# Kernel optimization log

Measured on AMD Instinct MI355X. Metric: run time of the kernel, lower is better.

## Reference

```python
import jax, jax.numpy as jnp
import numpy as np

N = 50000      # num nodes
E = 800000     # num edges (before self loops)
B = 50         # num graphs in batch
F_IN = 15
C = 64         # hidden_channels
H = 4          # num_heads
NEG_SLOPE = 0.2  # PyG GATConv default


def setup_inputs() -> dict:
    key = jax.random.key(0)
    ks = jax.random.split(key, 32)
    s = 0.05
    inp = {
        "x": jax.random.normal(ks[0], (N, F_IN), dtype=jnp.float32),
        "edge_index": jax.random.randint(ks[1], (2, E), 0, N, dtype=jnp.int32),
        "batch": jnp.sort(jax.random.randint(ks[2], (N,), 0, B, dtype=jnp.int32)),
        "W1": jax.random.normal(ks[3], (F_IN, H * C)) * s,
        "aS1": jax.random.normal(ks[4], (H, C)) * s,
        "aD1": jax.random.normal(ks[5], (H, C)) * s,
        "b1": jnp.zeros((H * C,)),
        "W2": jax.random.normal(ks[6], (H * C, H * C)) * s,
        "aS2": jax.random.normal(ks[7], (H, C)) * s,
        "aD2": jax.random.normal(ks[8], (H, C)) * s,
        "b2": jnp.zeros((H * C,)),
        # GAT layer 3: 256 -> 64, 1 head
        "W3": jax.random.normal(ks[9], (H * C, C)) * s,
        "aS3": jax.random.normal(ks[10], (1, C)) * s,
        "aD3": jax.random.normal(ks[11], (1, C)) * s,
        "b3": jnp.zeros((C,)),
        # node attention MLP: 64 -> 32 -> 1
        "Wna1": jax.random.normal(ks[12], (C, 32)) * s,
        "bna1": jnp.zeros((32,)),
        "Wna2": jax.random.normal(ks[13], (32, 1)) * s,
        "bna2": jnp.zeros((1,)),
        # graph classifier: 128 -> 128 -> 64 -> 1
        "Wc1": jax.random.normal(ks[14], (2 * C, 128)) * s,
        "bc1": jnp.zeros((128,)),
        "Wc2": jax.random.normal(ks[15], (128, 64)) * s,
        "bc2": jnp.zeros((64,)),
        "Wc3": jax.random.normal(ks[16], (64, 1)) * s,
        "bc3": jnp.zeros((1,)),
    }
    return inp


def _gat_conv(x, src, dst, W, a_src, a_dst, b, heads, ch):
    """PyG-style GATConv (add_self_loops=True, negative_slope=0.2, eval mode)."""
    n = x.shape[0]
    h = (x @ W).reshape(n, heads, ch)               # [N, H, C]
    alpha_s = jnp.einsum('nhc,hc->nh', h, a_src)    # per-node src score
    alpha_d = jnp.einsum('nhc,hc->nh', h, a_dst)
    loops = jnp.arange(n, dtype=src.dtype)
    s = jnp.concatenate([src, loops])               # [E+N]
    d = jnp.concatenate([dst, loops])
    e = jax.nn.leaky_relu(alpha_s[s] + alpha_d[d], NEG_SLOPE)   # [E+N, H]
    # segment softmax over incoming edges of each dst node
    m = jax.ops.segment_max(e, d, num_segments=n)
    ex = jnp.exp(e - m[d])
    denom = jax.ops.segment_sum(ex, d, num_segments=n)
    alpha = ex / denom[d]                           # [E+N, H]
    msg = h[s] * alpha[:, :, None]                  # [E+N, H, C]
    out = jax.ops.segment_sum(msg, d, num_segments=n)  # [N, H, C]
    return out.reshape(n, heads * ch) + b


def reference(x, edge_index, batch, W1, aS1, aD1, b1, W2, aS2, aD2, b2,
              W3, aS3, aD3, b3, Wna1, bna1, Wna2, bna2,
              Wc1, bc1, Wc2, bc2, Wc3, bc3):
    src, dst = edge_index[0], edge_index[1]
    x1 = jax.nn.elu(_gat_conv(x, src, dst, W1, aS1, aD1, b1, H, C))
    x2 = jax.nn.elu(_gat_conv(x1, src, dst, W2, aS2, aD2, b2, H, C))
    x3 = jax.nn.elu(_gat_conv(x2, src, dst, W3, aS3, aD3, b3, 1, C))  # [N, 64]

    # node attention: MLP then softmax over ALL nodes (dim=0, as in source)
    na = jax.nn.relu(x3 @ Wna1 + bna1) @ Wna2 + bna2   # [N, 1]
    node_attention = jax.nn.softmax(na, axis=0)

    # graph pooling
    ones = jnp.ones((x3.shape[0],), dtype=x3.dtype)
    cnt = jax.ops.segment_sum(ones, batch, num_segments=B)         # [B]
    mean = jax.ops.segment_sum(x3, batch, num_segments=B) / jnp.maximum(cnt, 1.0)[:, None]
    mx = jax.ops.segment_max(x3, batch, num_segments=B)
    mx = jnp.where(cnt[:, None] > 0, mx, 0.0)
    g = jnp.concatenate([mean, mx], axis=1)                        # [B, 128]

    h1 = jax.nn.relu(g @ Wc1 + bc1)
    h2 = jax.nn.relu(h1 @ Wc2 + bc2)
    risk = jax.nn.sigmoid(h2 @ Wc3 + bc3)                          # [B, 1]
    return (risk, node_attention)
```

## Files before the change

### kernel.cpp

```cpp
#include <hip/hip_runtime.h>
#include <math.h>

#define NN 50000
#define NP 50176
#define EE 800000
#define ETOT (EE + NN)
#define BB 50
#define PC 16

typedef unsigned short u16;
typedef unsigned char u8;
typedef __attribute__((ext_vector_type(8))) short short8;
typedef __attribute__((ext_vector_type(4))) float floatx4;
typedef __attribute__((ext_vector_type(2))) float floatx2;

__device__ __forceinline__ float b2f(u16 u) {
  return __int_as_float(((int)u) << 16);
}
__device__ __forceinline__ u16 f2b(float f) {
  unsigned u = __float_as_uint(f);
  unsigned r = (u + 0x7fffu + ((u >> 16) & 1u)) >> 16;
  return (u16)r;
}
__device__ __forceinline__ u8 f2f8(float v) {
  return (u8)(__builtin_amdgcn_cvt_pk_fp8_f32(v, v, 0, false) & 0xFF);
}
__device__ __forceinline__ float readlane_f(float v, int l) {
  return __int_as_float(__builtin_amdgcn_readlane(__float_as_int(v), l));
}
__device__ __forceinline__ float blo(unsigned w) { return __uint_as_float(w << 16); }
__device__ __forceinline__ float bhi(unsigned w) { return __uint_as_float(w & 0xffff0000u); }

__global__ void count_kernel(const int* __restrict__ ei, int* __restrict__ cnt) {
  int e = blockIdx.x * blockDim.x + threadIdx.x;
  if (e >= ETOT) return;
  int d = (e < EE) ? ei[EE + e] : (e - EE);
  atomicAdd(&cnt[d], 1);
}

__global__ void scan1_kernel(const int* __restrict__ cnt, int* __restrict__ rowp,
                             int* __restrict__ part) {
  __shared__ int s[512];
  int t = threadIdx.x;
  int i = blockIdx.x * 512 + t;
  int v = (i < NN) ? cnt[i] : 0;
  s[t] = v;
  __syncthreads();
  for (int off = 1; off < 512; off <<= 1) {
    int add = (t >= off) ? s[t - off] : 0;
    __syncthreads();
    s[t] += add;
    __syncthreads();
  }
  if (i < NN) rowp[i] = s[t] - v;
  if (t == 511) part[blockIdx.x] = s[511];
}

__global__ void scan2_kernel(int* __restrict__ part, int* __restrict__ rowp) {
  __shared__ int s[128];
  int t = threadIdx.x;
  int v = (t < 98) ? part[t] : 0;
  s[t] = v;
  __syncthreads();
  for (int off = 1; off < 128; off <<= 1) {
    int add = (t >= off) ? s[t - off] : 0;
    __syncthreads();
    s[t] += add;
    __syncthreads();
  }
  if (t < 98) part[t] = s[t] - v;
  if (t == 97) rowp[NN] = s[97];
}

__global__ void scan3_kernel(int* __restrict__ rowp, const int* __restrict__ part) {
  int i = blockIdx.x * 512 + threadIdx.x;
  if (i < NN) rowp[i] += part[blockIdx.x];
}

__global__ void fill_kernel(const int* __restrict__ ei, const int* __restrict__ rowp,
                            int* __restrict__ cur, int* __restrict__ col) {
  int e = blockIdx.x * blockDim.x + threadIdx.x;
  if (e >= ETOT) return;
  int s, d;
  if (e < EE) { s = ei[e]; d = ei[EE + e]; } else { s = e - EE; d = s; }
  int p = atomicAdd(&cur[d], 1);
  col[rowp[d] + p] = s;
}

__global__ void prep_kernel(const float* __restrict__ x, const float* __restrict__ W1,
                            const float* __restrict__ W2, const float* __restrict__ W3,
                            u16* __restrict__ xb, u16* __restrict__ W1t,
                            u16* __restrict__ W2t, u16* __restrict__ W3t) {
  const int T0 = NP * 32, T1 = T0 + 8192, T2 = T1 + 65536, T3 = T2 + 16384;
  int i = blockIdx.x * 256 + threadIdx.x;
  if (i < T0) {
    int n = i >> 5, c = i & 31;
    xb[i] = (n < NN && c < 15) ? f2b(x[n * 15 + c]) : (u16)0;
  } else if (i < T1) {
    int j = i - T0, n = j >> 5, k = j & 31;
    W1t[j] = (k < 15) ? f2b(W1[k * 256 + n]) : (u16)0;
  } else if (i < T2) {
    int j = i - T1, n = j >> 8, k = j & 255;
    W2t[j] = f2b(W2[k * 256 + n]);
  } else if (i < T3) {
    int j = i - T2, n = j >> 8, k = j & 255;
    W3t[j] = f2b(W3[k * 64 + n]);
  }
}

template <int BK, bool F8>
__global__ __launch_bounds__(256) void gemm_bf16_kernel(
    const u16* __restrict__ A, const u16* __restrict__ Bt, u16* __restrict__ C,
    u8* __restrict__ C8, int K, int N, const float* __restrict__ aS,
    const float* __restrict__ aD, float* __restrict__ as_o,
    float* __restrict__ ad_o, int Hh) {
  __shared__ u16 Al[128][BK + 8];
  __shared__ u16 Bl[64][BK + 8];
  __shared__ float sS[4][64], sD[4][64];
  int R0 = blockIdx.x * 128, C0 = blockIdx.y * 64;
  int wid = threadIdx.x >> 6, lane = threadIdx.x & 63;
  int wr = (wid >> 1) * 64, wc = (wid & 1) * 32;
  int lrow = lane & 15, lk8 = (lane >> 4) * 8;
  int rq = (lane >> 4) * 4;
  const int Q4 = BK / 4;
  const int nA = 128 * Q4, nB = 64 * Q4;
  floatx4 acc[4][2];
#pragma unroll
  for (int i = 0; i < 4; ++i)
#pragma unroll
    for (int j = 0; j < 2; ++j) acc[i][j] = (floatx4){0.f, 0.f, 0.f, 0.f};

  for (int k0 = 0; k0 < K; k0 += BK) {
    for (int c = threadIdx.x; c < nA + nB; c += 256) {
      if (c < nA) {
        int r = c / Q4, o = (c % Q4) * 4;
        *(ushort4*)&Al[r][o] = *(const ushort4*)&A[(size_t)(R0 + r) * K + k0 + o];
      } else {
        int c2 = c - nA;
        int r = c2 / Q4, o = (c2 % Q4) * 4;
        *(ushort4*)&Bl[r][o] = *(const ushort4*)&Bt[(size_t)(C0 + r) * K + k0 + o];
      }
    }
    __syncthreads();
#pragma unroll
    for (int ks = 0; ks < BK / 32; ++ks) {
      short8 a[4], b[2];
#pragma unroll
      for (int i = 0; i < 4; ++i) a[i] = *(const short8*)&Al[wr + i * 16 + lrow][ks * 32 + lk8];
#pragma unroll
      for (int j = 0; j < 2; ++j) b[j] = *(const short8*)&Bl[wc + j * 16 + lrow][ks * 32 + lk8];
#pragma unroll
      for (int i = 0; i < 4; ++i)
#pragma unroll
        for (int j = 0; j < 2; ++j)
          acc[i][j] = __builtin_amdgcn_mfma_f32_16x16x32_bf16(a[i], b[j], acc[i][j], 0, 0, 0);
    }
    __syncthreads();
  }
#pragma unroll
  for (int i = 0; i < 4; ++i)
#pragma unroll
    for (int j = 0; j < 2; ++j)
#pragma unroll
      for (int q = 0; q < 4; ++q) {
        int gr = R0 + wr + i * 16 + rq + q;
        int gc = C0 + wc + j * 16 + lrow;
        if constexpr (F8)
          C8[(size_t)gr * N + gc] = f2f8(acc[i][j][q]);
        else
          C[(size_t)gr * N + gc] = f2b(acc[i][j][q]);
      }
  int hb = blockIdx.y * 64;
  float wS0 = aS[hb + wc + lrow], wS1 = aS[hb + wc + 16 + lrow];
  float wD0 = aD[hb + wc + lrow], wD1 = aD[hb + wc + 16 + lrow];
#pragma unroll
  for (int i = 0; i < 4; ++i)
#pragma unroll
    for (int q = 0; q < 4; ++q) {
      float vS = acc[i][0][q] * wS0 + acc[i][1][q] * wS1;
      float vD = acc[i][0][q] * wD0 + acc[i][1][q] * wD1;
#pragma unroll
      for (int o = 8; o; o >>= 1) {
        vS += __shfl_xor(vS, o, 64);
        vD += __shfl_xor(vD, o, 64);
      }
      if (lrow == 0) {
        int rl = i * 16 + rq + q;
        sS[wid][rl] = vS;
        sD[wid][rl] = vD;
      }
    }
  __syncthreads();
  if (threadIdx.x < 128) {
    int p = threadIdx.x >> 6, r = threadIdx.x & 63;
    int gr = R0 + p * 64 + r;
    as_o[(size_t)gr * Hh + blockIdx.y] = sS[2 * p][r] + sS[2 * p + 1][r];
    ad_o[(size_t)gr * Hh + blockIdx.y] = sD[2 * p][r] + sD[2 * p + 1][r];
  }
}

__global__ __launch_bounds__(256) void agg4_kernel(
    const u8* __restrict__ h8, const float* __restrict__ as_i,
    const float* __restrict__ ad_i, const int* __restrict__ rowp,
    const int* __restrict__ col, const float* __restrict__ bias,
    u16* __restrict__ xo) {
  __shared__ float exs[4][64][4];
  int wid = threadIdx.x >> 6, lane = threadIdx.x & 63;
  int d = blockIdx.x * 4 + wid;
  int rp0 = rowp[d], deg = rowp[d + 1] - rp0;
  float4 add = *(const float4*)&ad_i[(size_t)d * 4];
  int hj = lane >> 4;
  int lq = lane << 2;
  float acc0 = 0.f, acc1 = 0.f, acc2 = 0.f, acc3 = 0.f;
  float den0 = 0.f, den1 = 0.f, den2 = 0.f, den3 = 0.f;

  for (int base = 0; base < deg; base += 64) {
    int i = base + lane;
    bool valid = i < deg;
    int s = valid ? col[rp0 + i] : 0;
    float4 asv = *(const float4*)&as_i[(size_t)s * 4];
    float e0 = asv.x + add.x, e1 = asv.y + add.y, e2 = asv.z + add.z, e3 = asv.w + add.w;
    e0 = (e0 > 0.f) ? e0 : 0.2f * e0;
    e1 = (e1 > 0.f) ? e1 : 0.2f * e1;
    e2 = (e2 > 0.f) ? e2 : 0.2f * e2;
    e3 = (e3 > 0.f) ? e3 : 0.2f * e3;
    float x0 = valid ? __expf(e0) : 0.f;
    float x1 = valid ? __expf(e1) : 0.f;
    float x2 = valid ? __expf(e2) : 0.f;
    float x3 = valid ? __expf(e3) : 0.f;
    den0 += x0; den1 += x1; den2 += x2; den3 += x3;
    *(float4*)&exs[wid][lane][0] = make_float4(x0, x1, x2, x3);
    __threadfence_block();
    int cnt = min(64, deg - base);
    int k8 = cnt & ~7;
    for (int k = 0; k < k8; k += 8) {
      unsigned wv[8];
      float qv[8];
#pragma unroll
      for (int u = 0; u < 8; ++u) {
        int sk = __builtin_amdgcn_readlane(s, k + u);
        qv[u] = exs[wid][k + u][hj];
        wv[u] = *(const unsigned*)&h8[(size_t)sk * 256 + lq];
      }
#pragma unroll
      for (int u = 0; u < 8; ++u) {
        floatx2 lo = __builtin_amdgcn_cvt_pk_f32_fp8(wv[u], false);
        floatx2 hi = __builtin_amdgcn_cvt_pk_f32_fp8(wv[u], true);
        acc0 += qv[u] * lo.x;
        acc1 += qv[u] * lo.y;
        acc2 += qv[u] * hi.x;
        acc3 += qv[u] * hi.y;
      }
    }
    for (int k = k8; k < cnt; ++k) {
      int sk = __builtin_amdgcn_readlane(s, k);
      float qk = exs[wid][k][hj];
      unsigned wv = *(const unsigned*)&h8[(size_t)sk * 256 + lq];
      floatx2 lo = __builtin_amdgcn_cvt_pk_f32_fp8(wv, false);
      floatx2 hi = __builtin_amdgcn_cvt_pk_f32_fp8(wv, true);
      acc0 += qk * lo.x;
      acc1 += qk * lo.y;
      acc2 += qk * hi.x;
      acc3 += qk * hi.y;
    }
  }
#pragma unroll
  for (int o = 32; o; o >>= 1) {
    den0 += __shfl_xor(den0, o, 64);
    den1 += __shfl_xor(den1, o, 64);
    den2 += __shfl_xor(den2, o, 64);
    den3 += __shfl_xor(den3, o, 64);
  }
  float den = (hj == 0) ? den0 : (hj == 1) ? den1 : (hj == 2) ? den2 : den3;
  float inv = 1.f / den;
  float4 bv = *(const float4*)&bias[lq];
  float v0 = acc0 * inv + bv.x;
  float v1 = acc1 * inv + bv.y;
  float v2 = acc2 * inv + bv.z;
  float v3 = acc3 * inv + bv.w;
  v0 = (v0 > 0.f) ? v0 : expm1f(v0);
  v1 = (v1 > 0.f) ? v1 : expm1f(v1);
  v2 = (v2 > 0.f) ? v2 : expm1f(v2);
  v3 = (v3 > 0.f) ? v3 : expm1f(v3);
  ushort4 o4;
  o4.x = f2b(v0); o4.y = f2b(v1); o4.z = f2b(v2); o4.w = f2b(v3);
  ((ushort4*)xo)[(size_t)d * 64 + lane] = o4;
}

__global__ __launch_bounds__(256) void agg1_kernel(
    const u16* __restrict__ h, const float* __restrict__ as_i,
    const float* __restrict__ ad_i, const int* __restrict__ rowp,
    const int* __restrict__ col, const float* __restrict__ bias,
    float* __restrict__ xo) {
  int wid = threadIdx.x >> 6, lane = threadIdx.x & 63;
  int d = blockIdx.x * 4 + wid;
  int rp0 = rowp[d], deg = rowp[d + 1] - rp0;
  float add = ad_i[d];
  float acc = 0.f, den = 0.f;
  for (int base = 0; base < deg; base += 64) {
    int i = base + lane;
    bool valid = i < deg;
    int s = valid ? col[rp0 + i] : 0;
    float e = as_i[s] + add;
    e = (e > 0.f) ? e : 0.2f * e;
    float ex = valid ? __expf(e) : 0.f;
    den += ex;
    int cnt = min(64, deg - base);
    int k8 = cnt & ~7;
    for (int k = 0; k < k8; k += 8) {
      int sA[8];
      float qA[8], hv[8];
#pragma unroll
      for (int u = 0; u < 8; ++u) {
        sA[u] = __builtin_amdgcn_readlane(s, k + u);
        qA[u] = readlane_f(ex, k + u);
      }
#pragma unroll
      for (int u = 0; u < 8; ++u) hv[u] = b2f(h[(size_t)sA[u] * 64 + lane]);
      float p0 = qA[0] * hv[0] + qA[1] * hv[1];
      float p1 = qA[2] * hv[2] + qA[3] * hv[3];
      float p2 = qA[4] * hv[4] + qA[5] * hv[5];
      float p3 = qA[6] * hv[6] + qA[7] * hv[7];
      acc += (p0 + p1) + (p2 + p3);
    }
    for (int k = k8; k < cnt; ++k) {
      int sk = __builtin_amdgcn_readlane(s, k);
      float qk = readlane_f(ex, k);
      acc += qk * b2f(h[(size_t)sk * 64 + lane]);
    }
  }
#pragma unroll
  for (int o = 32; o; o >>= 1) den += __shfl_xor(den, o, 64);
  float v = acc / den + bias[lane];
  v = (v > 0.f) ? v : expm1f(v);
  xo[(size_t)d * 64 + lane] = v;
}

__global__ void na_kernel(const float* __restrict__ x3, const float* __restrict__ W1,
                          const float* __restrict__ b1, const float* __restrict__ W2,
                          const float* __restrict__ b2, float* __restrict__ na,
                          float* __restrict__ gsum) {
  __shared__ float Ws[64 * 32];
  __shared__ float W2s[32];
  __shared__ float sred[4];
  for (int i = threadIdx.x; i < 2048; i += blockDim.x) Ws[i] = W1[i];
  if (threadIdx.x < 32) W2s[threadIdx.x] = W2[threadIdx.x];
  __syncthreads();
  int n = blockIdx.x * blockDim.x + threadIdx.x;
  float ez = 0.f;
  if (n < NN) {
    float hid[32];
#pragma unroll
    for (int j = 0; j < 32; ++j) hid[j] = b1[j];
    const float4* x4 = (const float4*)&x3[(size_t)n * 64];
    for (int kk = 0; kk < 16; ++kk) {
      float4 xv = x4[kk];
#pragma unroll
      for (int j = 0; j < 32; ++j) {
        hid[j] += xv.x * Ws[(kk * 4 + 0) * 32 + j];
        hid[j] += xv.y * Ws[(kk * 4 + 1) * 32 + j];
        hid[j] += xv.z * Ws[(kk * 4 + 2) * 32 + j];
        hid[j] += xv.w * Ws[(kk * 4 + 3) * 32 + j];
      }
    }
    float z = b2[0];
#pragma unroll
    for (int j = 0; j < 32; ++j) z += fmaxf(hid[j], 0.f) * W2s[j];
    ez = __expf(z);
    na[n] = ez;
  }
  float acc = ez;
  for (int o = 32; o; o >>= 1) acc += __shfl_xor(acc, o, 64);
  int wid = threadIdx.x >> 6, lane = threadIdx.x & 63;
  if (lane == 0) sred[wid] = acc;
  __syncthreads();
  if (threadIdx.x == 0) atomicAdd(gsum, sred[0] + sred[1] + sred[2] + sred[3]);
}

__global__ void na_write_kernel(const float* __restrict__ na, const float* __restrict__ gsum,
                                float* __restrict__ out) {
  int n = blockIdx.x * blockDim.x + threadIdx.x;
  if (n >= NN) return;
  out[n] = na[n] / gsum[0];
}

__global__ void pool1_kernel(const float* __restrict__ x3, const int* __restrict__ batch,
                             float* __restrict__ ppsum, float* __restrict__ ppmax) {
  int b = blockIdx.x, c = blockIdx.y;
  int lane = threadIdx.x & 63, wid = threadIdx.x >> 6;
  int lo = 0, hi = NN;
  while (lo < hi) { int m = (lo + hi) >> 1; if (batch[m] < b) lo = m + 1; else hi = m; }
  int start = lo;
  lo = start; hi = NN;
  while (lo < hi) { int m = (lo + hi) >> 1; if (batch[m] < b + 1) lo = m + 1; else hi = m; }
  int end = lo;
  int len = end - start;
  int c0 = start + (int)((long)len * c / PC);
  int c1 = start + (int)((long)len * (c + 1) / PC);
  float acc = 0.f, mx = -INFINITY;
  for (int n = c0 + wid; n < c1; n += 4) {
    float v = x3[(size_t)n * 64 + lane];
    acc += v;
    mx = fmaxf(mx, v);
  }
  __shared__ float ssum[4][64], smax[4][64];
  ssum[wid][lane] = acc;
  smax[wid][lane] = mx;
  __syncthreads();
  if (wid == 0) {
    acc = ssum[0][lane] + ssum[1][lane] + ssum[2][lane] + ssum[3][lane];
    mx = fmaxf(fmaxf(smax[0][lane], smax[1][lane]), fmaxf(smax[2][lane], smax[3][lane]));
    size_t o = ((size_t)c * BB + b) * 64 + lane;
    ppsum[o] = acc;
    ppmax[o] = mx;
  }
}

__global__ void pool2cls_kernel(const float* __restrict__ ppsum, const float* __restrict__ ppmax,
                                const int* __restrict__ batch, const float* __restrict__ Wc1,
                                const float* __restrict__ bc1, const float* __restrict__ Wc2,
                                const float* __restrict__ bc2, const float* __restrict__ Wc3,
                                const float* __restrict__ bc3, float* __restrict__ out) {
  __shared__ float g[128], h1[128], h2[64], scnt;
  int b = blockIdx.x, t = threadIdx.x;
  if (t == 0) {
    int lo = 0, hi = NN;
    while (lo < hi) { int m = (lo + hi) >> 1; if (batch[m] < b) lo = m + 1; else hi = m; }
    int start = lo;
    lo = start; hi = NN;
    while (lo < hi) { int m = (lo + hi) >> 1; if (batch[m] < b + 1) lo = m + 1; else hi = m; }
    scnt = (float)(lo - start);
  }
  float s = 0.f, m = -INFINITY;
  if (t < 64) {
#pragma unroll
    for (int c = 0; c < PC; ++c) {
      size_t o = ((size_t)c * BB + b) * 64 + t;
      s += ppsum[o];
      m = fmaxf(m, ppmax[o]);
    }
  }
  __syncthreads();
  float cnt = scnt;
  if (t < 64) {
    g[t] = (cnt > 0.f) ? s / fmaxf(cnt, 1.f) : 0.f;
    g[64 + t] = (cnt > 0.f) ? m : 0.f;
  }
  __syncthreads();
  float v = bc1[t];
  for (int k = 0; k < 128; ++k) v += g[k] * Wc1[k * 128 + t];
  h1[t] = fmaxf(v, 0.f);
  __syncthreads();
  if (t < 64) {
    float v2 = bc2[t];
    for (int k = 0; k < 128; ++k) v2 += h1[k] * Wc2[k * 64 + t];
    h2[t] = fmaxf(v2, 0.f);
  }
  __syncthreads();
  if (t == 0) {
    float z = bc3[0];
    for (int k = 0; k < 64; ++k) z += h2[k] * Wc3[k];
    out[b] = 1.f / (1.f + expf(-z));
  }
}

extern "C" void kernel_launch(void* const* d_in, const int* in_sizes, int n_in,
                              void* d_out, int out_size, void* d_ws, size_t ws_size,
                              hipStream_t stream) {
  const float* x    = (const float*)d_in[0];
  const int*   ei   = (const int*)d_in[1];
  const int*   batch= (const int*)d_in[2];
  const float* W1 = (const float*)d_in[3];
  const float* aS1= (const float*)d_in[4];
  const float* aD1= (const float*)d_in[5];
  const float* b1 = (const float*)d_in[6];
  const float* W2 = (const float*)d_in[7];
  const float* aS2= (const float*)d_in[8];
  const float* aD2= (const float*)d_in[9];
  const float* b2 = (const float*)d_in[10];
  const float* W3 = (const float*)d_in[11];
  const float* aS3= (const float*)d_in[12];
  const float* aD3= (const float*)d_in[13];
  const float* b3 = (const float*)d_in[14];
  const float* Wna1=(const float*)d_in[15];
  const float* bna1=(const float*)d_in[16];
  const float* Wna2=(const float*)d_in[17];
  const float* bna2=(const float*)d_in[18];
  const float* Wc1=(const float*)d_in[19];
  const float* bc1=(const float*)d_in[20];
  const float* Wc2=(const float*)d_in[21];
  const float* bc2=(const float*)d_in[22];
  const float* Wc3=(const float*)d_in[23];
  const float* bc3=(const float*)d_in[24];
  float* out = (float*)d_out;

  char* w = (char*)d_ws;
  size_t off = 0;
  auto alloc = [&](size_t bytes) {
    void* p = w + off;
    off = (off + bytes + 255) & ~(size_t)255;
    return p;
  };
  u16* xb   = (u16*)alloc((size_t)NP * 32 * 2);
  u16* bufA = (u16*)alloc((size_t)NP * 256 * 2);
  u16* bufB = (u16*)alloc((size_t)NP * 256 * 2);
  u8*  h8   = (u8*)alloc((size_t)NP * 256);
  u16* W1t  = (u16*)alloc((size_t)256 * 32 * 2);
  u16* W2t  = (u16*)alloc((size_t)256 * 256 * 2);
  u16* W3t  = (u16*)alloc((size_t)64 * 256 * 2);
  float* asb  = (float*)alloc((size_t)NP * 4 * 4);
  float* adb  = (float*)alloc((size_t)NP * 4 * 4);
  float* nab  = (float*)alloc((size_t)NN * 4);
  int* rowp = (int*)alloc((size_t)(NN + 1) * 4);
  int* cntb = (int*)alloc((size_t)NN * 4);
  int* curb = (int*)alloc((size_t)NN * 4);
  float* gsum = (float*)alloc(256);
  size_t zspan = (size_t)((char*)gsum + 256 - (char*)cntb);
  int* colb = (int*)alloc((size_t)ETOT * 4);
  int* part = (int*)alloc(128 * 4);
  float* ppsum = (float*)alloc((size_t)PC * BB * 64 * 4);
  float* ppmax = (float*)alloc((size_t)PC * BB * 64 * 4);
  float* x3 = (float*)bufB;
  (void)ws_size; (void)in_sizes; (void)n_in; (void)out_size;

  hipMemsetAsync(cntb, 0, zspan, stream);

  count_kernel<<<(ETOT + 255) / 256, 256, 0, stream>>>(ei, cntb);
  scan1_kernel<<<98, 512, 0, stream>>>(cntb, rowp, part);
  scan2_kernel<<<1, 128, 0, stream>>>(part, rowp);
  scan3_kernel<<<98, 512, 0, stream>>>(rowp, part);
  fill_kernel<<<(ETOT + 255) / 256, 256, 0, stream>>>(ei, rowp, curb, colb);

  const int PREP_TOT = NP * 32 + 8192 + 65536 + 16384;
  prep_kernel<<<(PREP_TOT + 255) / 256, 256, 0, stream>>>(x, W1, W2, W3, xb, W1t, W2t, W3t);

  const int GX = NP / 128;
  gemm_bf16_kernel<32, true><<<dim3(GX, 4), 256, 0, stream>>>(
      xb, W1t, nullptr, h8, 32, 256, aS1, aD1, asb, adb, 4);
  agg4_kernel<<<12500, 256, 0, stream>>>(h8, asb, adb, rowp, colb, b1, bufB);
  gemm_bf16_kernel<64, true><<<dim3(GX, 4), 256, 0, stream>>>(
      bufB, W2t, nullptr, h8, 256, 256, aS2, aD2, asb, adb, 4);
  agg4_kernel<<<12500, 256, 0, stream>>>(h8, asb, adb, rowp, colb, b2, bufB);
  gemm_bf16_kernel<64, false><<<dim3(GX, 1), 256, 0, stream>>>(
      bufB, W3t, bufA, nullptr, 256, 64, aS3, aD3, asb, adb, 1);
  agg1_kernel<<<12500, 256, 0, stream>>>(bufA, asb, adb, rowp, colb, b3, x3);

  na_kernel<<<(NN + 255) / 256, 256, 0, stream>>>(x3, Wna1, bna1, Wna2, bna2, nab, gsum);
  na_write_kernel<<<(NN + 255) / 256, 256, 0, stream>>>(nab, gsum, out + BB);

  pool1_kernel<<<dim3(BB, PC), 256, 0, stream>>>(x3, batch, ppsum, ppmax);
  pool2cls_kernel<<<BB, 128, 0, stream>>>(ppsum, ppmax, batch, Wc1, bc1, Wc2, bc2,
                                          Wc3, bc3, out);
}
```

Before: 375.0 us.

## Widen GEMM tiles, split edge aggregation across waves, fuse node-attention MLP into agg1

GEMM for layers 1-2 now uses 128x128 tiles with two heads per block and writes attention scores directly, halving block count and redundant A loads. The 4-head aggregation assigns two wavefronts per destination node, each handling half the edges, then combines partials through shared memory. Tail loops are replaced with padded 8-wide batches. The node-attention MLP is fused into the final aggregation kernel, removing a separate pass over x3. This trades more LDS use and larger blocks for more memory-level parallelism on the gathers.

After: 542.0 us. 44.5% more time.

```diff
diff --git a/kernel.cpp b/kernel.cpp
--- a/kernel.cpp
+++ b/kernel.cpp
@@ -28,8 +28,6 @@
 __device__ __forceinline__ float readlane_f(float v, int l) {
   return __int_as_float(__builtin_amdgcn_readlane(__float_as_int(v), l));
 }
-__device__ __forceinline__ float blo(unsigned w) { return __uint_as_float(w << 16); }
-__device__ __forceinline__ float bhi(unsigned w) { return __uint_as_float(w & 0xffff0000u); }
 
 __global__ void count_kernel(const int* __restrict__ ei, int* __restrict__ cnt) {
   int e = blockIdx.x * blockDim.x + threadIdx.x;
@@ -108,16 +106,100 @@
   }
 }
 
-template <int BK, bool F8>
-__global__ __launch_bounds__(256) void gemm_bf16_kernel(
+template <int BK>
+__global__ __launch_bounds__(256) void gemm128_kernel(
+    const u16* __restrict__ A, const u16* __restrict__ Bt, u8* __restrict__ C8,
+    int K, const float* __restrict__ aS, const float* __restrict__ aD,
+    float* __restrict__ as_o, float* __restrict__ ad_o) {
+  __shared__ u16 Al[128][BK + 8];
+  __shared__ u16 Bl[128][BK + 8];
+  int R0 = blockIdx.x * 128, C0 = blockIdx.y * 128;
+  int wid = threadIdx.x >> 6, lane = threadIdx.x & 63;
+  int wr = (wid >> 1) * 64, wc = (wid & 1) * 64;
+  int lrow = lane & 15, lk8 = (lane >> 4) * 8;
+  int rq = (lane >> 4) * 4;
+  const int Q4 = BK / 4;
+  const int nA = 128 * Q4;
+  floatx4 acc[4][4];
+#pragma unroll
+  for (int i = 0; i < 4; ++i)
+#pragma unroll
+    for (int j = 0; j < 4; ++j) acc[i][j] = (floatx4){0.f, 0.f, 0.f, 0.f};
+
+  for (int k0 = 0; k0 < K; k0 += BK) {
+    for (int c = threadIdx.x; c < 2 * nA; c += 256) {
+      if (c < nA) {
+        int r = c / Q4, o = (c % Q4) * 4;
+        *(ushort4*)&Al[r][o] = *(const ushort4*)&A[(size_t)(R0 + r) * K + k0 + o];
+      } else {
+        int c2 = c - nA;
+        int r = c2 / Q4, o = (c2 % Q4) * 4;
+        *(ushort4*)&Bl[r][o] = *(const ushort4*)&Bt[(size_t)(C0 + r) * K + k0 + o];
+      }
+    }
+    __syncthreads();
+#pragma unroll
+    for (int ks = 0; ks < BK / 32; ++ks) {
+      short8 a[4], b[4];
+#pragma unroll
+      for (int i = 0; i < 4; ++i) a[i] = *(const short8*)&Al[wr + i * 16 + lrow][ks * 32 + lk8];
+#pragma unroll
+      for (int j = 0; j < 4; ++j) b[j] = *(const short8*)&Bl[wc + j * 16 + lrow][ks * 32 + lk8];
+#pragma unroll
+      for (int i = 0; i < 4; ++i)
+#pragma unroll
+        for (int j = 0; j < 4; ++j)
+          acc[i][j] = __builtin_amdgcn_mfma_f32_16x16x32_bf16(a[i], b[j], acc[i][j], 0, 0, 0);
+    }
+    __syncthreads();
+  }
+#pragma unroll
+  for (int i = 0; i < 4; ++i)
+#pragma unroll
+    for (int j = 0; j < 4; ++j)
+#pragma unroll
+      for (int q = 0; q < 4; ++q) {
+        int gr = R0 + wr + i * 16 + rq + q;
+        int gc = C0 + wc + j * 16 + lrow;
+        C8[(size_t)gr * 256 + gc] = f2f8(acc[i][j][q]);
+      }
+  int hb = blockIdx.y * 2 + (wid & 1);
+  float wS[4], wD[4];
+#pragma unroll
+  for (int j = 0; j < 4; ++j) {
+    wS[j] = aS[hb * 64 + j * 16 + lrow];
+    wD[j] = aD[hb * 64 + j * 16 + lrow];
+  }
+#pragma unroll
+  for (int i = 0; i < 4; ++i)
+#pragma unroll
+    for (int q = 0; q < 4; ++q) {
+      float vS = acc[i][0][q] * wS[0] + acc[i][1][q] * wS[1] +
+                 acc[i][2][q] * wS[2] + acc[i][3][q] * wS[3];
+      float vD = acc[i][0][q] * wD[0] + acc[i][1][q] * wD[1] +
+                 acc[i][2][q] * wD[2] + acc[i][3][q] * wD[3];
+#pragma unroll
+      for (int o = 8; o; o >>= 1) {
+        vS += __shfl_xor(vS, o, 64);
+        vD += __shfl_xor(vD, o, 64);
+      }
+      if (lrow == 0) {
+        int gr = R0 + wr + i * 16 + rq + q;
+        as_o[(size_t)gr * 4 + hb] = vS;
+        ad_o[(size_t)gr * 4 + hb] = vD;
+      }
+    }
+}
+
+__global__ __launch_bounds__(256) void gemm64_kernel(
     const u16* __restrict__ A, const u16* __restrict__ Bt, u16* __restrict__ C,
-    u8* __restrict__ C8, int K, int N, const float* __restrict__ aS,
-    const float* __restrict__ aD, float* __restrict__ as_o,
-    float* __restrict__ ad_o, int Hh) {
+    int K, const float* __restrict__ aS, const float* __restrict__ aD,
+    float* __restrict__ as_o, float* __restrict__ ad_o) {
+  const int BK = 64;
   __shared__ u16 Al[128][BK + 8];
   __shared__ u16 Bl[64][BK + 8];
   __shared__ float sS[4][64], sD[4][64];
-  int R0 = blockIdx.x * 128, C0 = blockIdx.y * 64;
+  int R0 = blockIdx.x * 128;
   int wid = threadIdx.x >> 6, lane = threadIdx.x & 63;
   int wr = (wid >> 1) * 64, wc = (wid & 1) * 32;
   int lrow = lane & 15, lk8 = (lane >> 4) * 8;
@@ -138,7 +220,7 @@
       } else {
         int c2 = c - nA;
         int r = c2 / Q4, o = (c2 % Q4) * 4;
-        *(ushort4*)&Bl[r][o] = *(const ushort4*)&Bt[(size_t)(C0 + r) * K + k0 + o];
+        *(ushort4*)&Bl[r][o] = *(const ushort4*)&Bt[(size_t)r * K + k0 + o];
       }
     }
     __syncthreads();
@@ -164,15 +246,10 @@
 #pragma unroll
       for (int q = 0; q < 4; ++q) {
         int gr = R0 + wr + i * 16 + rq + q;
-        int gc = C0 + wc + j * 16 + lrow;
-        if constexpr (F8)
-          C8[(size_t)gr * N + gc] = f2f8(acc[i][j][q]);
-        else
-          C[(size_t)gr * N + gc] = f2b(acc[i][j][q]);
-      }
-  int hb = blockIdx.y * 64;
-  float wS0 = aS[hb + wc + lrow], wS1 = aS[hb + wc + 16 + lrow];
-  float wD0 = aD[hb + wc + lrow], wD1 = aD[hb + wc + 16 + lrow];
+        C[(size_t)gr * 64 + wc + j * 16 + lrow] = f2b(acc[i][j][q]);
+      }
+  float wS0 = aS[wc + lrow], wS1 = aS[wc + 16 + lrow];
+  float wD0 = aD[wc + lrow], wD1 = aD[wc + 16 + lrow];
 #pragma unroll
   for (int i = 0; i < 4; ++i)
 #pragma unroll
@@ -194,29 +271,61 @@
   if (threadIdx.x < 128) {
     int p = threadIdx.x >> 6, r = threadIdx.x & 63;
     int gr = R0 + p * 64 + r;
-    as_o[(size_t)gr * Hh + blockIdx.y] = sS[2 * p][r] + sS[2 * p + 1][r];
-    ad_o[(size_t)gr * Hh + blockIdx.y] = sD[2 * p][r] + sD[2 * p + 1][r];
-  }
-}
-
-__global__ __launch_bounds__(256) void agg4_kernel(
+    as_o[gr] = sS[2 * p][r] + sS[2 * p + 1][r];
+    ad_o[gr] = sD[2 * p][r] + sD[2 * p + 1][r];
+  }
+}
+
+template <int B>
+__device__ __forceinline__ void agg4_batch(
+    const u8* __restrict__ h8, int s, int kbase, int cnt, int hj, int lq,
+    const float (*__restrict__ exsw)[4], float& a0, float& a1, float& a2, float& a3) {
+  unsigned wv[B];
+  float qv[B];
+#pragma unroll
+  for (int u = 0; u < B; ++u) {
+    int ke = kbase + u;
+    int kc = (ke < cnt) ? ke : (cnt - 1);
+    int sk = __builtin_amdgcn_readlane(s, kc);
+    qv[u] = (ke < cnt) ? exsw[kc][hj] : 0.f;
+    wv[u] = *(const unsigned*)&h8[(size_t)sk * 256 + lq];
+  }
+#pragma unroll
+  for (int u = 0; u < B; ++u) {
+    floatx2 lo = __builtin_amdgcn_cvt_pk_f32_fp8(wv[u], false);
+    floatx2 hi = __builtin_amdgcn_cvt_pk_f32_fp8(wv[u], true);
+    a0 += qv[u] * lo.x;
+    a1 += qv[u] * lo.y;
+    a2 += qv[u] * hi.x;
+    a3 += qv[u] * hi.y;
+  }
+}
+
+__global__ __launch_bounds__(512) void agg4_kernel(
     const u8* __restrict__ h8, const float* __restrict__ as_i,
     const float* __restrict__ ad_i, const int* __restrict__ rowp,
     const int* __restrict__ col, const float* __restrict__ bias,
     u16* __restrict__ xo) {
-  __shared__ float exs[4][64][4];
+  __shared__ float exs[8][64][4];
+  __shared__ float4 accb[8][64];
+  __shared__ float denb[8][4];
   int wid = threadIdx.x >> 6, lane = threadIdx.x & 63;
-  int d = blockIdx.x * 4 + wid;
+  int half = wid & 1, dslot = wid >> 1;
+  int d = blockIdx.x * 4 + dslot;
   int rp0 = rowp[d], deg = rowp[d + 1] - rp0;
+  int mid = deg >> 1;
+  int lo_e = half ? mid : 0;
+  int hi_e = half ? deg : mid;
   float4 add = *(const float4*)&ad_i[(size_t)d * 4];
   int hj = lane >> 4;
   int lq = lane << 2;
-  float acc0 = 0.f, acc1 = 0.f, acc2 = 0.f, acc3 = 0.f;
+  const float(*exsw)[4] = exs[wid];
+  float a0 = 0.f, a1 = 0.f, a2 = 0.f, a3 = 0.f;
   float den0 = 0.f, den1 = 0.f, den2 = 0.f, den3 = 0.f;
 
-  for (int base = 0; base < deg; base += 64) {
+  for (int base = lo_e; base < hi_e; base += 64) {
     int i = base + lane;
-    bool valid = i < deg;
+    bool valid = i < hi_e;
     int s = valid ? col[rp0 + i] : 0;
     float4 asv = *(const float4*)&as_i[(size_t)s * 4];
     float e0 = asv.x + add.x, e1 = asv.y + add.y, e2 = asv.z + add.z, e3 = asv.w + add.w;
@@ -231,38 +340,9 @@
     den0 += x0; den1 += x1; den2 += x2; den3 += x3;
     *(float4*)&exs[wid][lane][0] = make_float4(x0, x1, x2, x3);
     __threadfence_block();
-    int cnt = min(64, deg - base);
-    int k8 = cnt & ~7;
-    for (int k = 0; k < k8; k += 8) {
-      unsigned wv[8];
-      float qv[8];
-#pragma unroll
-      for (int u = 0; u < 8; ++u) {
-        int sk = __builtin_amdgcn_readlane(s, k + u);
-        qv[u] = exs[wid][k + u][hj];
-        wv[u] = *(const unsigned*)&h8[(size_t)sk * 256 + lq];
-      }
-#pragma unroll
-      for (int u = 0; u < 8; ++u) {
-        floatx2 lo = __builtin_amdgcn_cvt_pk_f32_fp8(wv[u], false);
-        floatx2 hi = __builtin_amdgcn_cvt_pk_f32_fp8(wv[u], true);
-        acc0 += qv[u] * lo.x;
-        acc1 += qv[u] * lo.y;
-        acc2 += qv[u] * hi.x;
-        acc3 += qv[u] * hi.y;
-      }
-    }
-    for (int k = k8; k < cnt; ++k) {
-      int sk = __builtin_amdgcn_readlane(s, k);
-      float qk = exs[wid][k][hj];
-      unsigned wv = *(const unsigned*)&h8[(size_t)sk * 256 + lq];
-      floatx2 lo = __builtin_amdgcn_cvt_pk_f32_fp8(wv, false);
-      floatx2 hi = __builtin_amdgcn_cvt_pk_f32_fp8(wv, true);
-      acc0 += qk * lo.x;
-      acc1 += qk * lo.y;
-      acc2 += qk * hi.x;
-      acc3 += qk * hi.y;
-    }
+    int cnt = min(64, hi_e - base);
+    for (int kb = 0; kb < cnt; kb += 8)
+      agg4_batch<8>(h8, s, kb, cnt, hj, lq, exsw, a0, a1, a2, a3);
   }
 #pragma unroll
   for (int o = 32; o; o >>= 1) {
@@ -271,27 +351,68 @@
     den2 += __shfl_xor(den2, o, 64);
     den3 += __shfl_xor(den3, o, 64);
   }
-  float den = (hj == 0) ? den0 : (hj == 1) ? den1 : (hj == 2) ? den2 : den3;
-  float inv = 1.f / den;
-  float4 bv = *(const float4*)&bias[lq];
-  float v0 = acc0 * inv + bv.x;
-  float v1 = acc1 * inv + bv.y;
-  float v2 = acc2 * inv + bv.z;
-  float v3 = acc3 * inv + bv.w;
-  v0 = (v0 > 0.f) ? v0 : expm1f(v0);
-  v1 = (v1 > 0.f) ? v1 : expm1f(v1);
-  v2 = (v2 > 0.f) ? v2 : expm1f(v2);
-  v3 = (v3 > 0.f) ? v3 : expm1f(v3);
-  ushort4 o4;
-  o4.x = f2b(v0); o4.y = f2b(v1); o4.z = f2b(v2); o4.w = f2b(v3);
-  ((ushort4*)xo)[(size_t)d * 64 + lane] = o4;
-}
-
-__global__ __launch_bounds__(256) void agg1_kernel(
+  accb[wid][lane] = make_float4(a0, a1, a2, a3);
+  if (lane == 0) {
+    denb[wid][0] = den0; denb[wid][1] = den1;
+    denb[wid][2] = den2; denb[wid][3] = den3;
+  }
+  __syncthreads();
+  if (half == 0) {
+    float4 p = accb[wid ^ 1][lane];
+    a0 += p.x; a1 += p.y; a2 += p.z; a3 += p.w;
+    den0 += denb[wid ^ 1][0];
+    den1 += denb[wid ^ 1][1];
+    den2 += denb[wid ^ 1][2];
+    den3 += denb[wid ^ 1][3];
+    float den = (hj == 0) ? den0 : (hj == 1) ? den1 : (hj == 2) ? den2 : den3;
+    float inv = 1.f / den;
+    float4 bv = *(const float4*)&bias[lq];
+    float v0 = a0 * inv + bv.x;
+    float v1 = a1 * inv + bv.y;
+    float v2 = a2 * inv + bv.z;
+    float v3 = a3 * inv + bv.w;
+    v0 = (v0 > 0.f) ? v0 : expm1f(v0);
+    v1 = (v1 > 0.f) ? v1 : expm1f(v1);
+    v2 = (v2 > 0.f) ? v2 : expm1f(v2);
+    v3 = (v3 > 0.f) ? v3 : expm1f(v3);
+    ushort4 o4;
+    o4.x = f2b(v0); o4.y = f2b(v1); o4.z = f2b(v2); o4.w = f2b(v3);
+    ((ushort4*)xo)[(size_t)d * 64 + lane] = o4;
+  }
+}
+
+template <int B>
+__device__ __forceinline__ void agg1_batch(
+    const u16* __restrict__ h, int s, int kbase, int cnt, int lane, float ex,
+    float& acc) {
+  float hv[B], qv[B];
+#pragma unroll
+  for (int u = 0; u < B; ++u) {
+    int ke = kbase + u;
+    int kc = (ke < cnt) ? ke : (cnt - 1);
+    int sk = __builtin_amdgcn_readlane(s, kc);
+    qv[u] = (ke < cnt) ? readlane_f(ex, kc) : 0.f;
+    hv[u] = b2f(h[(size_t)sk * 64 + lane]);
+  }
+#pragma unroll
+  for (int u = 0; u < B; ++u) acc += qv[u] * hv[u];
+}
+
+__global__ __launch_bounds__(256) void agg1na_kernel(
     const u16* __restrict__ h, const float* __restrict__ as_i,
     const float* __restrict__ ad_i, const int* __restrict__ rowp,
     const int* __restrict__ col, const float* __restrict__ bias,
-    float* __restrict__ xo) {
+    float* __restrict__ xo, const float* __restrict__ Wna1,
+    const float* __restrict__ bna1, const float* __restrict__ Wna2,
+    const float* __restrict__ bna2, float* __restrict__ na,
+    float* __restrict__ gsum) {
+  __shared__ float Ws[2048];
+  __shared__ float W2s[32];
+  __shared__ float xrow[4][64];
+  __shared__ float sred[4];
+  for (int i = threadIdx.x; i < 2048; i += 256) Ws[i] = Wna1[i];
+  if (threadIdx.x < 32) W2s[threadIdx.x] = Wna2[threadIdx.x];
+  __syncthreads();
   int wid = threadIdx.x >> 6, lane = threadIdx.x & 63;
   int d = blockIdx.x * 4 + wid;
   int rp0 = rowp[d], deg = rowp[d + 1] - rp0;
@@ -306,73 +427,28 @@
     float ex = valid ? __expf(e) : 0.f;
     den += ex;
     int cnt = min(64, deg - base);
-    int k8 = cnt & ~7;
-    for (int k = 0; k < k8; k += 8) {
-      int sA[8];
-      float qA[8], hv[8];
-#pragma unroll
-      for (int u = 0; u < 8; ++u) {
-        sA[u] = __builtin_amdgcn_readlane(s, k + u);
-        qA[u] = readlane_f(ex, k + u);
-      }
-#pragma unroll
-      for (int u = 0; u < 8; ++u) hv[u] = b2f(h[(size_t)sA[u] * 64 + lane]);
-      float p0 = qA[0] * hv[0] + qA[1] * hv[1];
-      float p1 = qA[2] * hv[2] + qA[3] * hv[3];
-      float p2 = qA[4] * hv[4] + qA[5] * hv[5];
-      float p3 = qA[6] * hv[6] + qA[7] * hv[7];
-      acc += (p0 + p1) + (p2 + p3);
-    }
-    for (int k = k8; k < cnt; ++k) {
-      int sk = __builtin_amdgcn_readlane(s, k);
-      float qk = readlane_f(ex, k);
-      acc += qk * b2f(h[(size_t)sk * 64 + lane]);
-    }
+    for (int kb = 0; kb < cnt; kb += 8)
+      agg1_batch<8>(h, s, kb, cnt, lane, ex, acc);
   }
 #pragma unroll
   for (int o = 32; o; o >>= 1) den += __shfl_xor(den, o, 64);
   float v = acc / den + bias[lane];
   v = (v > 0.f) ? v : expm1f(v);
   xo[(size_t)d * 64 + lane] = v;
-}
-
-__global__ void na_kernel(const float* __restrict__ x3, const float* __restrict__ W1,
-                          const float* __restrict__ b1, const float* __restrict__ W2,
-                          const float* __restrict__ b2, float* __restrict__ na,
-                          float* __restrict__ gsum) {
-  __shared__ float Ws[64 * 32];
-  __shared__ float W2s[32];
-  __shared__ float sred[4];
-  for (int i = threadIdx.x; i < 2048; i += blockDim.x) Ws[i] = W1[i];
-  if (threadIdx.x < 32) W2s[threadIdx.x] = W2[threadIdx.x];
-  __syncthreads();
-  int n = blockIdx.x * blockDim.x + threadIdx.x;
-  float ez = 0.f;
-  if (n < NN) {
-    float hid[32];
-#pragma unroll
-    for (int j = 0; j < 32; ++j) hid[j] = b1[j];
-    const float4* x4 = (const float4*)&x3[(size_t)n * 64];
-    for (int kk = 0; kk < 16; ++kk) {
-      float4 xv = x4[kk];
-#pragma unroll
-      for (int j = 0; j < 32; ++j) {
-        hid[j] += xv.x * Ws[(kk * 4 + 0) * 32 + j];
-        hid[j] += xv.y * Ws[(kk * 4 + 1) * 32 + j];
-        hid[j] += xv.z * Ws[(kk * 4 + 2) * 32 + j];
-        hid[j] += xv.w * Ws[(kk * 4 + 3) * 32 + j];
-      }
-    }
-    float z = b2[0];
-#pragma unroll
-    for (int j = 0; j < 32; ++j) z += fmaxf(hid[j], 0.f) * W2s[j];
-    ez = __expf(z);
-    na[n] = ez;
-  }
-  float acc = ez;
-  for (int o = 32; o; o >>= 1) acc += __shfl_xor(acc, o, 64);
-  int wid = threadIdx.x >> 6, lane = threadIdx.x & 63;
-  if (lane == 0) sred[wid] = acc;
+  xrow[wid][lane] = v;
+  __threadfence_block();
+  int j = lane & 31;
+  int coff = (lane >> 5) * 32;
+  float hj = 0.f;
+#pragma unroll
+  for (int c = 0; c < 32; ++c) hj += xrow[wid][coff + c] * Ws[(coff + c) * 32 + j];
+  hj += __shfl_xor(hj, 32, 64);
+  hj += bna1[j];
+  float r = fmaxf(hj, 0.f) * W2s[j];
+#pragma unroll
+  for (int o = 16; o; o >>= 1) r += __shfl_xor(r, o, 64);
+  float ez = __expf(r + bna2[0]);
+  if (lane == 0) { na[d] = ez; sred[wid] = ez; }
   __syncthreads();
   if (threadIdx.x == 0) atomicAdd(gsum, sred[0] + sred[1] + sred[2] + sred[3]);
 }
@@ -535,19 +611,15 @@
   prep_kernel<<<(PREP_TOT + 255) / 256, 256, 0, stream>>>(x, W1, W2, W3, xb, W1t, W2t, W3t);
 
   const int GX = NP / 128;
-  gemm_bf16_kernel<32, true><<<dim3(GX, 4), 256, 0, stream>>>(
-      xb, W1t, nullptr, h8, 32, 256, aS1, aD1, asb, adb, 4);
-  agg4_kernel<<<12500, 256, 0, stream>>>(h8, asb, adb, rowp, colb, b1, bufB);
-  gemm_bf16_kernel<64, true><<<dim3(GX, 4), 256, 0, stream>>>(
-      bufB, W2t, nullptr, h8, 256, 256, aS2, aD2, asb, adb, 4);
-  agg4_kernel<<<12500, 256, 0, stream>>>(h8, asb, adb, rowp, colb, b2, bufB);
-  gemm_bf16_kernel<64, false><<<dim3(GX, 1), 256, 0, stream>>>(
-      bufB, W3t, bufA, nullptr, 256, 64, aS3, aD3, asb, adb, 1);
-  agg1_kernel<<<12500, 256, 0, stream>>>(bufA, asb, adb, rowp, colb, b3, x3);
-
-  na_kernel<<<(NN + 255) / 256, 256, 0, stream>>>(x3, Wna1, bna1, Wna2, bna2, nab, gsum);
+  gemm128_kernel<32><<<dim3(GX, 2), 256, 0, stream>>>(xb, W1t, h8, 32, aS1, aD1, asb, adb);
+  agg4_kernel<<<12500, 512, 0, stream>>>(h8, asb, adb, rowp, colb, b1, bufB);
+  gemm128_kernel<64><<<dim3(GX, 2), 256, 0, stream>>>(bufB, W2t, h8, 256, aS2, aD2, asb, adb);
+  agg4_kernel<<<12500, 512, 0, stream>>>(h8, asb, adb, rowp, colb, b2, bufB);
+  gemm64_kernel<<<GX, 256, 0, stream>>>(bufB, W3t, bufA, 256, aS3, aD3, asb, adb);
+  agg1na_kernel<<<12500, 256, 0, stream>>>(bufA, asb, adb, rowp, colb, b3, x3,
+                                           Wna1, bna1, Wna2, bna2, nab, gsum);
+
   na_write_kernel<<<(NN + 255) / 256, 256, 0, stream>>>(nab, gsum, out + BB);
-
   pool1_kernel<<<dim3(BB, PC), 256, 0, stream>>>(x3, batch, ppsum, ppmax);
   pool2cls_kernel<<<BB, 128, 0, stream>>>(ppsum, ppmax, batch, Wc1, bc1, Wc2, bc2,
                                           Wc3, bc3, out);
```
